# Kernel tuning notes

Hardware: AMD Instinct MI355X
Metric: run time of the kernel (lower is better)

The kernel has to match this reference:

```python
import jax, jax.numpy as jnp
import numpy as np

B, N, PREV, PRED, H = 16, 64, 6, 30, 256
E = N * (N - 1)
BN_EPS = 1e-5


def _mlp(x, W1, b1, W2, b2, gamma, beta):
    # Two-layer ELU MLP with batch norm over flattened (batch*rows) dim.
    h = jax.nn.elu(x @ W1 + b1)
    h = jax.nn.elu(h @ W2 + b2)
    b, n, d = h.shape
    f = h.reshape(b * n, d)
    mu = f.mean(axis=0)
    var = f.var(axis=0)
    f = (f - mu) * jax.lax.rsqrt(var + BN_EPS) * gamma + beta
    return f.reshape(b, n, d)


def setup_inputs() -> dict:
    key = jax.random.key(0)
    ks = jax.random.split(key, 8)
    # fully-connected directed graph without self loops
    recv, send = np.where(~np.eye(N, dtype=bool))  # each [E]
    rel_rec = jnp.broadcast_to(jax.nn.one_hot(jnp.asarray(recv), N)[None], (B, E, N)).astype(jnp.float32)
    rel_send = jnp.broadcast_to(jax.nn.one_hot(jnp.asarray(send), N)[None], (B, E, N)).astype(jnp.float32)

    def xavier(k, shape):
        fan_in, fan_out = shape
        std = np.sqrt(2.0 / (fan_in + fan_out))
        return jax.random.normal(k, shape, jnp.float32) * std

    return {
        "prev_actor_centers": jax.random.normal(ks[0], (B, N, PREV, 2), jnp.float32) * 10.0,
        "rel_rec": rel_rec,
        "rel_send": rel_send,
        "W_traj": xavier(ks[1], (PREV * 2, H)),
        "b_traj": jnp.full((H,), 0.1, jnp.float32),
        "n2e_W1": xavier(ks[2], (2 * H, H)),
        "n2e_b1": jnp.full((H,), 0.1, jnp.float32),
        "n2e_W2": xavier(ks[3], (H, H)),
        "n2e_b2": jnp.full((H,), 0.1, jnp.float32),
        "n2e_gamma": jnp.ones((H,), jnp.float32),
        "n2e_beta": jnp.zeros((H,), jnp.float32),
        "e2n_W1": xavier(ks[4], (2 * H, H)),
        "e2n_b1": jnp.full((H,), 0.1, jnp.float32),
        "e2n_W2": xavier(ks[5], (H, H)),
        "e2n_b2": jnp.full((H,), 0.1, jnp.float32),
        "e2n_gamma": jnp.ones((H,), jnp.float32),
        "e2n_beta": jnp.zeros((H,), jnp.float32),
        "W_fuse": xavier(ks[6], (2 * H, H)),
        "b_fuse": jnp.full((H,), 0.1, jnp.float32),
        "W_pred": xavier(ks[7], (H, PRED * 2)),
        "b_pred": jnp.full((PRED * 2,), 0.1, jnp.float32),
    }


def reference(prev_actor_centers, rel_rec, rel_send,
              W_traj, b_traj,
              n2e_W1, n2e_b1, n2e_W2, n2e_b2, n2e_gamma, n2e_beta,
              e2n_W1, e2n_b1, e2n_W2, e2n_b2, e2n_gamma, e2n_beta,
              W_fuse, b_fuse, W_pred, b_pred):
    b, n, prev, _ = prev_actor_centers.shape
    # relative displacements, first step zero
    diffs = prev_actor_centers[:, :, 1:, :] - prev_actor_centers[:, :, :-1, :]
    rel_pos = jnp.concatenate([jnp.zeros((b, n, 1, 2), prev_actor_centers.dtype), diffs], axis=2)
    rel_pos = rel_pos.reshape(b, n, prev * 2)
    x = rel_pos @ W_traj + b_traj  # [b, n, H] node features

    # node2edge: gather via one-hot relation matmuls
    receivers = jnp.einsum('ben,bnh->beh', rel_rec, x)
    senders = jnp.einsum('ben,bnh->beh', rel_send, x)
    edges = jnp.concatenate([receivers, senders], axis=-1)  # [b, E, 2H]
    e = _mlp(edges, n2e_W1, n2e_b1, n2e_W2, n2e_b2, n2e_gamma, n2e_beta)

    # edge2node: degree-normalized scatter via transposed relation matmuls
    deg_rec = rel_rec.sum(axis=1)  # [b, n]
    deg_rec = deg_rec + (deg_rec == 0).astype(deg_rec.dtype)
    incoming = jnp.einsum('ben,beh->bnh', rel_rec, e) / deg_rec[..., None]
    deg_send = rel_send.sum(axis=1)
    deg_send = deg_send + (deg_send == 0).astype(deg_send.dtype)
    outgoing = jnp.einsum('ben,beh->bnh', rel_send, e) / deg_send[..., None]
    nodes = jnp.concatenate([incoming, outgoing], axis=-1)  # [b, n, 2H]
    m = _mlp(nodes, e2n_W1, e2n_b1, e2n_W2, e2n_b2, e2n_gamma, e2n_beta)

    fused = jnp.concatenate([x, m], axis=-1) @ W_fuse + b_fuse  # [b, n, H]
    rel = fused @ W_pred + b_pred  # [b, n, PRED*2]

    current_loc = prev_actor_centers[:, :, -1, :]  # [b, n, 2]
    current_loc = jnp.broadcast_to(current_loc[:, :, None, :], (b, n, PRED, 2)).reshape(b, n, PRED * 2)
    pos = jnp.cumsum(rel.reshape(b, n, PRED, 2), axis=2).reshape(b, n, PRED * 2) + current_loc
    return (rel, pos)
```

## Files before the change

kernel.cpp:

```cpp
#include <hip/hip_runtime.h>
#include <hip/hip_bf16.h>

#define BB 16
#define NN 64
#define PREVN 6
#define PREDN 30
#define HH 256
#define EE 4032
#define EROWS (BB*EE)
#define NROWS (BB*NN)

typedef short short8 __attribute__((ext_vector_type(8)));
typedef float f32x4 __attribute__((ext_vector_type(4)));

enum : int {
  OFF_STATS_E = 0,
  OFF_STATS_M = 1024,
  OFF_XRS     = 2048,
  F32_END     = 264192
};
enum : size_t {
  BO_W1TE  = 0,
  BO_W2TE  = 131072,
  BO_W1TN  = 196608,
  BO_W2TN  = 327680,
  BO_WFT   = 393216,
  BO_WPT   = 524288,
  BO_XG    = 540672,
  BO_NODES = 802816,
  BO_H1G   = 1327104,
  BO_M2    = 1589248,
  BO_FG    = 1851392,
  BO_E2    = 2113536
};

__device__ __forceinline__ float eluf(float v) { return v > 0.f ? v : __expf(v) - 1.f; }

__device__ __forceinline__ float xembed(const float* __restrict__ centers,
                                        const float* __restrict__ Wt,
                                        const float* __restrict__ bt,
                                        int rr, int col) {
  const float* c = centers + rr * 12;
  float acc = bt[col];
  #pragma unroll
  for (int t = 0; t < 5; ++t) {
    float dx = c[(t+1)*2 + 0] - c[t*2 + 0];
    float dy = c[(t+1)*2 + 1] - c[t*2 + 1];
    acc += dx * Wt[(2 + 2*t)*HH + col] + dy * Wt[(3 + 2*t)*HH + col];
  }
  return acc;
}

struct PrepArgs {
  const float *centers, *W_traj, *b_traj;
  const float *n2e_W1, *n2e_W2, *e2n_W1, *e2n_W2, *W_fuse, *W_pred;
  float* ws;
  __hip_bfloat16 *w1te, *w2te, *w1tn, *w2tn, *wft, *wpt, *xg;
};

__global__ __launch_bounds__(256) void k_prep(PrepArgs a) {
  __shared__ float t[64][65];
  const int bid = blockIdx.x, tid = threadIdx.x;
  if (bid < 128) {
    const float* W; __hip_bfloat16* WT; int K, lb;
    if (bid < 32)      { W = a.n2e_W1; WT = a.w1te; K = 512; lb = bid; }
    else if (bid < 48) { W = a.n2e_W2; WT = a.w2te; K = 256; lb = bid - 32; }
    else if (bid < 80) { W = a.e2n_W1; WT = a.w1tn; K = 512; lb = bid - 48; }
    else if (bid < 96) { W = a.e2n_W2; WT = a.w2tn; K = 256; lb = bid - 80; }
    else               { W = a.W_fuse; WT = a.wft;  K = 512; lb = bid - 96; }
    int KB = K / 64;
    int k0 = (lb % KB) * 64, n0 = (lb / KB) * 64;
    int tx = tid & 63, ty = tid >> 6;
    #pragma unroll
    for (int i = 0; i < 16; ++i)
      t[ty + i*4][tx] = W[(size_t)(k0 + ty + i*4) * 256 + n0 + tx];
    __syncthreads();
    #pragma unroll
    for (int i = 0; i < 16; ++i)
      WT[(size_t)(n0 + ty + i*4) * K + k0 + tx] = __float2bfloat16(t[tx][ty + i*4]);
  } else if (bid < 192) {
    int idx = (bid - 128) * 256 + tid;
    int c = idx >> 8, k = idx & 255;
    a.wpt[idx] = __float2bfloat16(c < 60 ? a.W_pred[k * 60 + c] : 0.f);
  } else if (bid < 200) {
    a.ws[(bid - 192) * 256 + tid] = 0.f;
  } else {
    int row0 = (bid - 200) * 16;
    #pragma unroll
    for (int r = 0; r < 16; ++r)
      a.xg[(size_t)(row0 + r)*256 + tid] =
          __float2bfloat16(xembed(a.centers, a.W_traj, a.b_traj, row0 + r, tid));
  }
}

__global__ __launch_bounds__(64) void k_xrs2(
    const __hip_bfloat16* __restrict__ xg,
    const __hip_bfloat16* __restrict__ W1T,
    const float* __restrict__ b1,
    __hip_bfloat16* __restrict__ xrs) {
  const int lane = threadIdx.x;
  const int m16 = lane & 15, quad = lane >> 4;
  const int ko = quad * 8;
  const int rt = blockIdx.x >> 3, s = blockIdx.x & 7;
  const int half = s >> 2, j0 = (s & 3) * 64;
  const int row0 = rt * 16;
  __hip_bfloat16* dst = xrs + (size_t)half * 262144;

  f32x4 acc[4];
  #pragma unroll
  for (int jt = 0; jt < 4; ++jt) {
    float bv = half ? 0.f : b1[j0 + jt*16 + m16];
    acc[jt] = (f32x4){bv, bv, bv, bv};
  }
  #pragma unroll
  for (int ks = 0; ks < 8; ++ks) {
    short8 af = *reinterpret_cast<const short8*>(
        xg + (size_t)(row0 + m16)*256 + ks*32 + ko);
    short8 bf[4];
    #pragma unroll
    for (int jt = 0; jt < 4; ++jt)
      bf[jt] = *reinterpret_cast<const short8*>(
          W1T + (size_t)(j0 + jt*16 + m16)*512 + half*256 + ks*32 + ko);
    #pragma unroll
    for (int jt = 0; jt < 4; ++jt)
      acc[jt] = __builtin_amdgcn_mfma_f32_16x16x32_bf16(af, bf[jt], acc[jt], 0, 0, 0);
  }
  #pragma unroll
  for (int jt = 0; jt < 4; ++jt)
    #pragma unroll
    for (int r = 0; r < 4; ++r)
      dst[(size_t)(row0 + quad*4 + r)*256 + j0 + jt*16 + m16] =
          __float2bfloat16(acc[jt][r]);
}

__global__ __launch_bounds__(256, 4) void k_mlp6(
    const __hip_bfloat16* __restrict__ xrs,
    const __hip_bfloat16* __restrict__ W2T,
    const float* __restrict__ b2,
    __hip_bfloat16* __restrict__ outp,
    float* __restrict__ stats) {
  __shared__ alignas(16) __hip_bfloat16 h1s[64][264];
  __shared__ float sst[2][256];
  __shared__ int sd64[64];
  __shared__ int rcf[64];
  const int tid = threadIdx.x;
  const int w = tid >> 6, lane = tid & 63;
  const int m16 = lane & 15, quad = lane >> 4;
  const int ko = quad * 8;
  const int blk = blockIdx.x;
  const int bb = blk / 63, lb = blk - bb*63;
  const int row0 = blk * 64;
  const int n0 = (lb * 64) / 63;
  const int colw = w * 64;

  if (tid < 64) {
    int e = lb*64 + tid;
    int rc = e / 63; int jj = e - rc*63;
    sd64[tid] = jj + (jj >= rc ? 1 : 0);
    rcf[tid]  = rc - n0;
  }
  sst[0][tid] = 0.f;
  sst[1][tid] = 0.f;
  __syncthreads();

  {
    const int ty = tid >> 7;
    const int c2 = (tid & 127) * 2;
    const __hip_bfloat16* xrb = xrs + (size_t)(bb*64 + n0)*256 + c2;
    const __hip_bfloat16* xsb = xrs + 262144 + (size_t)bb*64*256 + c2;
    #pragma unroll 4
    for (int r2 = 0; r2 < 32; ++r2) {
      int r = ty*32 + r2;
      __hip_bfloat162 xa = *reinterpret_cast<const __hip_bfloat162*>(
          xrb + (size_t)rcf[r]*256);
      __hip_bfloat162 xs2 = *reinterpret_cast<const __hip_bfloat162*>(
          xsb + (size_t)sd64[r]*256);
      __hip_bfloat162 o;
      o.x = __float2bfloat16(eluf(__bfloat162float(xa.x) + __bfloat162float(xs2.x)));
      o.y = __float2bfloat16(eluf(__bfloat162float(xa.y) + __bfloat162float(xs2.y)));
      *reinterpret_cast<__hip_bfloat162*>(&h1s[r][c2]) = o;
    }
  }
  __syncthreads();

  f32x4 acc2[4][4];
  #pragma unroll
  for (int jt = 0; jt < 4; ++jt) {
    float bv = b2[colw + jt*16 + m16];
    #pragma unroll
    for (int mt = 0; mt < 4; ++mt) acc2[mt][jt] = (f32x4){bv, bv, bv, bv};
  }
  #pragma unroll
  for (int kt = 0; kt < 4; ++kt) {
    #pragma unroll
    for (int ks = 0; ks < 2; ++ks) {
      const int k0 = kt*64 + ks*32 + ko;
      short8 af[4], bf[4];
      #pragma unroll
      for (int jt = 0; jt < 4; ++jt)
        bf[jt] = *reinterpret_cast<const short8*>(
            W2T + (size_t)(colw + jt*16 + m16)*256 + k0);
      #pragma unroll
      for (int mt = 0; mt < 4; ++mt)
        af[mt] = *(const short8*)((const char*)h1s +
                     (size_t)(mt*16 + m16)*528 + k0*2);
      #pragma unroll
      for (int mt = 0; mt < 4; ++mt)
        #pragma unroll
        for (int jt = 0; jt < 4; ++jt)
          acc2[mt][jt] = __builtin_amdgcn_mfma_f32_16x16x32_bf16(af[mt], bf[jt],
                                                                 acc2[mt][jt], 0, 0, 0);
    }
  }
  __syncthreads();

  #pragma unroll
  for (int jt = 0; jt < 4; ++jt) {
    float ps = 0.f, pq = 0.f;
    #pragma unroll
    for (int mt = 0; mt < 4; ++mt)
      #pragma unroll
      for (int r = 0; r < 4; ++r) {
        float hv = eluf(acc2[mt][jt][r]);
        h1s[mt*16 + quad*4 + r][colw + jt*16 + m16] = __float2bfloat16(hv);
        ps += hv; pq += hv * hv;
      }
    atomicAdd(&sst[0][colw + jt*16 + m16], ps);
    atomicAdd(&sst[1][colw + jt*16 + m16], pq);
  }
  __syncthreads();

  atomicAdd(&stats[tid], sst[0][tid]);
  atomicAdd(&stats[256 + tid], sst[1][tid]);
  #pragma unroll
  for (int i = 0; i < 8; ++i) {
    int u = i*256 + tid;
    int r = u >> 5, c = (u & 31) * 8;
    *reinterpret_cast<uint4*>(outp + (size_t)(row0 + r)*HH + c) =
        *reinterpret_cast<const uint4*>(&h1s[r][c]);
  }
}

__global__ __launch_bounds__(1024) void k_agg2(const __hip_bfloat16* __restrict__ e2,
                                               const float* __restrict__ st,
                                               const float* __restrict__ gam,
                                               const float* __restrict__ bet,
                                               __hip_bfloat16* __restrict__ nodes) {
  __shared__ float red[32][256];
  const int blk = blockIdx.x;
  const int bn = blk >> 1, half = blk & 1;
  const int b = bn >> 6, n = bn & 63;
  const int tid = threadIdx.x;
  const int c8 = (tid & 31) * 8;
  const int rg = tid >> 5;
  const __hip_bfloat16* base = e2 + (size_t)b * EE * HH;
  float s[8] = {0.f,0.f,0.f,0.f,0.f,0.f,0.f,0.f};
  for (int j = rg; j < 63; j += 32) {
    const __hip_bfloat16* rp;
    if (half == 0) {
      rp = base + (size_t)(n*63 + j)*HH;
    } else {
      int i = j + (j >= n ? 1 : 0);
      int e = i*63 + n - (n > i ? 1 : 0);
      rp = base + (size_t)e*HH;
    }
    union { uint4 u; __hip_bfloat16 h[8]; } v;
    v.u = *reinterpret_cast<const uint4*>(rp + c8);
    #pragma unroll
    for (int jj = 0; jj < 8; ++jj) s[jj] += __bfloat162float(v.h[jj]);
  }
  #pragma unroll
  for (int jj = 0; jj < 8; jj += 4)
    *reinterpret_cast<float4*>(&red[rg][c8 + jj]) =
        (float4){s[jj], s[jj+1], s[jj+2], s[jj+3]};
  __syncthreads();
  if (tid < 256) {
    float S = 0.f;
    #pragma unroll
    for (int r = 0; r < 32; ++r) S += red[r][tid];
    const float inv = 1.f / (float)EROWS;
    float mean = st[tid] * inv;
    float var  = fmaxf(st[256 + tid] * inv - mean*mean, 0.f);
    float a = gam[tid] * rsqrtf(var + 1e-5f);
    float c0 = bet[tid] - mean * a;
    nodes[(size_t)bn*512 + half*256 + tid] = __float2bfloat16(a * S * (1.f/63.f) + c0);
  }
}

__global__ __launch_bounds__(64) void k_n1(
    const __hip_bfloat16* __restrict__ nodes,
    const __hip_bfloat16* __restrict__ W1T,
    const float* __restrict__ b1,
    __hip_bfloat16* __restrict__ h1g) {
  __shared__ alignas(16) __hip_bfloat16 hls[16][40];
  const int lane = threadIdx.x;
  const int m16 = lane & 15, quad = lane >> 4;
  const int ko = quad * 8;
  const int row0 = (blockIdx.x >> 3) * 16;
  const int j0 = (blockIdx.x & 7) * 32;

  f32x4 acc[2];
  #pragma unroll
  for (int jt = 0; jt < 2; ++jt) {
    float bv = b1[j0 + jt*16 + m16];
    acc[jt] = (f32x4){bv, bv, bv, bv};
  }
  #pragma unroll
  for (int ks = 0; ks < 16; ++ks) {
    short8 af = *reinterpret_cast<const short8*>(
        nodes + (size_t)(row0 + m16)*512 + ks*32 + ko);
    short8 bf[2];
    #pragma unroll
    for (int jt = 0; jt < 2; ++jt)
      bf[jt] = *reinterpret_cast<const short8*>(
          W1T + (size_t)(j0 + jt*16 + m16)*512 + ks*32 + ko);
    #pragma unroll
    for (int jt = 0; jt < 2; ++jt)
      acc[jt] = __builtin_amdgcn_mfma_f32_16x16x32_bf16(af, bf[jt], acc[jt], 0, 0, 0);
  }
  #pragma unroll
  for (int jt = 0; jt < 2; ++jt)
    #pragma unroll
    for (int r = 0; r < 4; ++r)
      hls[quad*4 + r][jt*16 + m16] = __float2bfloat16(eluf(acc[jt][r]));
  {
    int r = lane >> 2, c = (lane & 3) * 8;
    *reinterpret_cast<uint4*>(h1g + (size_t)(row0 + r)*256 + j0 + c) =
        *reinterpret_cast<const uint4*>(&hls[r][c]);
  }
}

__global__ __launch_bounds__(64) void k_n2(
    const __hip_bfloat16* __restrict__ h1g,
    const __hip_bfloat16* __restrict__ W2T,
    const float* __restrict__ b2,
    __hip_bfloat16* __restrict__ m2,
    float* __restrict__ stats) {
  __shared__ alignas(16) __hip_bfloat16 hls[16][40];
  __shared__ float sst[2][32];
  const int lane = threadIdx.x;
  const int m16 = lane & 15, quad = lane >> 4;
  const int ko = quad * 8;
  const int row0 = (blockIdx.x >> 3) * 16;
  const int j0 = (blockIdx.x & 7) * 32;

  if (lane < 32) { sst[0][lane] = 0.f; sst[1][lane] = 0.f; }

  f32x4 acc[2];
  #pragma unroll
  for (int jt = 0; jt < 2; ++jt) {
    float bv = b2[j0 + jt*16 + m16];
    acc[jt] = (f32x4){bv, bv, bv, bv};
  }
  #pragma unroll
  for (int ks = 0; ks < 8; ++ks) {
    short8 af = *reinterpret_cast<const short8*>(
        h1g + (size_t)(row0 + m16)*256 + ks*32 + ko);
    short8 bf[2];
    #pragma unroll
    for (int jt = 0; jt < 2; ++jt)
      bf[jt] = *reinterpret_cast<const short8*>(
          W2T + (size_t)(j0 + jt*16 + m16)*256 + ks*32 + ko);
    #pragma unroll
    for (int jt = 0; jt < 2; ++jt)
      acc[jt] = __builtin_amdgcn_mfma_f32_16x16x32_bf16(af, bf[jt], acc[jt], 0, 0, 0);
  }
  #pragma unroll
  for (int jt = 0; jt < 2; ++jt) {
    float ps = 0.f, pq = 0.f;
    #pragma unroll
    for (int r = 0; r < 4; ++r) {
      float hv = eluf(acc[jt][r]);
      hls[quad*4 + r][jt*16 + m16] = __float2bfloat16(hv);
      ps += hv; pq += hv * hv;
    }
    atomicAdd(&sst[0][jt*16 + m16], ps);
    atomicAdd(&sst[1][jt*16 + m16], pq);
  }
  if (lane < 32) {
    atomicAdd(&stats[j0 + lane], sst[0][lane]);
    atomicAdd(&stats[256 + j0 + lane], sst[1][lane]);
  }
  {
    int r = lane >> 2, c = (lane & 3) * 8;
    *reinterpret_cast<uint4*>(m2 + (size_t)(row0 + r)*256 + j0 + c) =
        *reinterpret_cast<const uint4*>(&hls[r][c]);
  }
}

__global__ __launch_bounds__(64) void k_hf(
    const __hip_bfloat16* __restrict__ xg,
    const __hip_bfloat16* __restrict__ m2,
    const float* __restrict__ stM,
    const float* __restrict__ gam,
    const float* __restrict__ bet,
    const __hip_bfloat16* __restrict__ WfT,
    const float* __restrict__ bfv,
    __hip_bfloat16* __restrict__ fg) {
  __shared__ alignas(16) __hip_bfloat16 hls[16][40];
  __shared__ float bnA[256], bnC[256];
  const int lane = threadIdx.x;
  const int m16 = lane & 15, quad = lane >> 4;
  const int ko = quad * 8;
  const int row0 = (blockIdx.x >> 3) * 16;
  const int j0 = (blockIdx.x & 7) * 32;

  {
    const float inv = 1.f / (float)NROWS;
    #pragma unroll
    for (int j = 0; j < 4; ++j) {
      int k = lane*4 + j;
      float mean = stM[k] * inv;
      float var  = fmaxf(stM[256 + k] * inv - mean*mean, 0.f);
      float am = gam[k] * rsqrtf(var + 1e-5f);
      bnA[k] = am;
      bnC[k] = bet[k] - mean * am;
    }
  }

  f32x4 acc[2];
  #pragma unroll
  for (int jt = 0; jt < 2; ++jt) {
    float bv = bfv[j0 + jt*16 + m16];
    acc[jt] = (f32x4){bv, bv, bv, bv};
  }
  #pragma unroll
  for (int ks = 0; ks < 16; ++ks) {
    short8 af;
    if (ks < 8) {
      af = *reinterpret_cast<const short8*>(
          xg + (size_t)(row0 + m16)*256 + ks*32 + ko);
    } else {
      int k0 = (ks - 8)*32 + ko;
      union { uint4 u; __hip_bfloat16 h[8]; } v;
      v.u = *reinterpret_cast<const uint4*>(m2 + (size_t)(row0 + m16)*256 + k0);
      union { short8 s8; __hip_bfloat16 h[8]; } o;
      #pragma unroll
      for (int j = 0; j < 8; ++j)
        o.h[j] = __float2bfloat16(bnA[k0+j] * __bfloat162float(v.h[j]) + bnC[k0+j]);
      af = o.s8;
    }
    short8 bf[2];
    #pragma unroll
    for (int jt = 0; jt < 2; ++jt)
      bf[jt] = *reinterpret_cast<const short8*>(
          WfT + (size_t)(j0 + jt*16 + m16)*512 + ks*32 + ko);
    #pragma unroll
    for (int jt = 0; jt < 2; ++jt)
      acc[jt] = __builtin_amdgcn_mfma_f32_16x16x32_bf16(af, bf[jt], acc[jt], 0, 0, 0);
  }
  #pragma unroll
  for (int jt = 0; jt < 2; ++jt)
    #pragma unroll
    for (int r = 0; r < 4; ++r)
      hls[quad*4 + r][jt*16 + m16] = __float2bfloat16(acc[jt][r]);
  {
    int r = lane >> 2, c = (lane & 3) * 8;
    *reinterpret_cast<uint4*>(fg + (size_t)(row0 + r)*256 + j0 + c) =
        *reinterpret_cast<const uint4*>(&hls[r][c]);
  }
}

__global__ __launch_bounds__(64) void k_pred(
    const __hip_bfloat16* __restrict__ fg,
    const __hip_bfloat16* __restrict__ WpT,
    const float* __restrict__ bp,
    const float* __restrict__ centers,
    float* __restrict__ out) {
  __shared__ float rl[16][68];
  const int lane = threadIdx.x;
  const int m16 = lane & 15, quad = lane >> 4;
  const int ko = quad * 8;
  const int row0 = blockIdx.x * 16;

  f32x4 acc[4];
  #pragma unroll
  for (int jt = 0; jt < 4; ++jt) {
    int c = jt*16 + m16;
    float bv = (c < 60) ? bp[c] : 0.f;
    acc[jt] = (f32x4){bv, bv, bv, bv};
  }
  #pragma unroll
  for (int ks = 0; ks < 8; ++ks) {
    short8 af = *reinterpret_cast<const short8*>(
        fg + (size_t)(row0 + m16)*256 + ks*32 + ko);
    short8 bf[4];
    #pragma unroll
    for (int jt = 0; jt < 4; ++jt)
      bf[jt] = *reinterpret_cast<const short8*>(
          WpT + (size_t)(jt*16 + m16)*256 + ks*32 + ko);
    #pragma unroll
    for (int jt = 0; jt < 4; ++jt)
      acc[jt] = __builtin_amdgcn_mfma_f32_16x16x32_bf16(af, bf[jt], acc[jt], 0, 0, 0);
  }
  #pragma unroll
  for (int jt = 0; jt < 4; ++jt) {
    int c = jt*16 + m16;
    #pragma unroll
    for (int r = 0; r < 4; ++r) {
      int lr = quad*4 + r;
      rl[lr][c] = acc[jt][r];
      if (c < 60) out[(size_t)(row0 + lr)*60 + c] = acc[jt][r];
    }
  }
  if (lane < 32) {
    int lr = lane >> 1, xy = lane & 1;
    int grow = row0 + lr;
    float run = centers[(size_t)(grow*PREVN + 5)*2 + xy];
    #pragma unroll
    for (int p = 0; p < PREDN; ++p) {
      run += rl[lr][2*p + xy];
      out[61440 + (size_t)grow*60 + 2*p + xy] = run;
    }
  }
}

extern "C" void kernel_launch(void* const* d_in, const int* in_sizes, int n_in,
                              void* d_out, int out_size, void* d_ws, size_t ws_size,
                              hipStream_t stream) {
  const float* centers = (const float*)d_in[0];
  float* ws = (float*)d_ws;
  __hip_bfloat16* wb = (__hip_bfloat16*)(ws + F32_END);
  __hip_bfloat16* xrs = (__hip_bfloat16*)(ws + OFF_XRS);

  const float* W_traj = (const float*)d_in[3];
  const float* b_traj = (const float*)d_in[4];
  const float* n2e_b1 = (const float*)d_in[6];
  const float* n2e_b2 = (const float*)d_in[8];
  const float* n2e_g  = (const float*)d_in[9];
  const float* n2e_be = (const float*)d_in[10];
  const float* e2n_b1 = (const float*)d_in[12];
  const float* e2n_b2 = (const float*)d_in[14];
  const float* e2n_g  = (const float*)d_in[15];
  const float* e2n_be = (const float*)d_in[16];
  const float* b_fuse = (const float*)d_in[18];
  const float* b_pred = (const float*)d_in[20];

  PrepArgs pa;
  pa.centers = centers; pa.W_traj = W_traj; pa.b_traj = b_traj;
  pa.n2e_W1 = (const float*)d_in[5];  pa.n2e_W2 = (const float*)d_in[7];
  pa.e2n_W1 = (const float*)d_in[11]; pa.e2n_W2 = (const float*)d_in[13];
  pa.W_fuse = (const float*)d_in[17]; pa.W_pred = (const float*)d_in[19];
  pa.ws = ws;
  pa.w1te = wb + BO_W1TE; pa.w2te = wb + BO_W2TE;
  pa.w1tn = wb + BO_W1TN; pa.w2tn = wb + BO_W2TN;
  pa.wft = wb + BO_WFT;   pa.wpt = wb + BO_WPT;
  pa.xg = wb + BO_XG;

  k_prep<<<264, 256, 0, stream>>>(pa);
  k_xrs2<<<512, 64, 0, stream>>>(wb + BO_XG, wb + BO_W1TE, n2e_b1, xrs);
  k_mlp6<<<EROWS/64, 256, 0, stream>>>(xrs, wb + BO_W2TE, n2e_b2, wb + BO_E2,
                                       ws + OFF_STATS_E);
  k_agg2<<<2*NROWS, 1024, 0, stream>>>(wb + BO_E2, ws + OFF_STATS_E, n2e_g, n2e_be,
                                       wb + BO_NODES);
  k_n1<<<512, 64, 0, stream>>>(wb + BO_NODES, wb + BO_W1TN, e2n_b1, wb + BO_H1G);
  k_n2<<<512, 64, 0, stream>>>(wb + BO_H1G, wb + BO_W2TN, e2n_b2, wb + BO_M2,
                               ws + OFF_STATS_M);
  k_hf<<<512, 64, 0, stream>>>(wb + BO_XG, wb + BO_M2, ws + OFF_STATS_M,
                               e2n_g, e2n_be, wb + BO_WFT, b_fuse, wb + BO_FG);
  k_pred<<<64, 64, 0, stream>>>(wb + BO_FG, wb + BO_WPT, b_pred, centers,
                                (float*)d_out);
}
```

Baseline: 200.0 us.

## Fuse incoming-edge aggregation into edge MLP epilogue and vectorize gather

Edge blocks in the edge-MLP kernel now keep per-receiver partial sums of their outputs, split at the boundary between the two receiver nodes each 64-row tile covers. These are atomically added into a zeroed fp32 buffer, so the aggregation kernel only gathers the strided sender-side rows and uses smaller blocks. The h1 gather also changes from bf16x2 loads with index tables in shared memory to uint4 loads with indices computed inline. The cost is extra global atomics plus a zeroing pass in the prep kernel. The buffer is aliased onto the H1G region, which is written later.

```diff
diff --git a/kernel.cpp b/kernel.cpp
--- a/kernel.cpp
+++ b/kernel.cpp
@@ -55,6 +55,7 @@
   const float *centers, *W_traj, *b_traj;
   const float *n2e_W1, *n2e_W2, *e2n_W1, *e2n_W2, *W_fuse, *W_pred;
   float* ws;
+  float* inc;
   __hip_bfloat16 *w1te, *w2te, *w1tn, *w2tn, *wft, *wpt, *xg;
 };
 
@@ -84,12 +85,17 @@
     a.wpt[idx] = __float2bfloat16(c < 60 ? a.W_pred[k * 60 + c] : 0.f);
   } else if (bid < 200) {
     a.ws[(bid - 192) * 256 + tid] = 0.f;
-  } else {
+  } else if (bid < 264) {
     int row0 = (bid - 200) * 16;
     #pragma unroll
     for (int r = 0; r < 16; ++r)
       a.xg[(size_t)(row0 + r)*256 + tid] =
           __float2bfloat16(xembed(a.centers, a.W_traj, a.b_traj, row0 + r, tid));
+  } else {
+    float* p = a.inc + (size_t)(bid - 264) * 4096;
+    #pragma unroll
+    for (int i = 0; i < 4; ++i)
+      *reinterpret_cast<float4*>(p + (i*256 + tid)*4) = (float4){0.f,0.f,0.f,0.f};
   }
 }
 
@@ -133,16 +139,15 @@
           __float2bfloat16(acc[jt][r]);
 }
 
-__global__ __launch_bounds__(256, 4) void k_mlp6(
+__global__ __launch_bounds__(256, 4) void k_mlp7(
     const __hip_bfloat16* __restrict__ xrs,
     const __hip_bfloat16* __restrict__ W2T,
     const float* __restrict__ b2,
     __hip_bfloat16* __restrict__ outp,
-    float* __restrict__ stats) {
+    float* __restrict__ stats,
+    float* __restrict__ incraw) {
   __shared__ alignas(16) __hip_bfloat16 h1s[64][264];
-  __shared__ float sst[2][256];
-  __shared__ int sd64[64];
-  __shared__ int rcf[64];
+  __shared__ float sst[3][256];
   const int tid = threadIdx.x;
   const int w = tid >> 6, lane = tid & 63;
   const int m16 = lane & 15, quad = lane >> 4;
@@ -151,34 +156,35 @@
   const int bb = blk / 63, lb = blk - bb*63;
   const int row0 = blk * 64;
   const int n0 = (lb * 64) / 63;
+  const int thr = (n0 + 1) * 63 - lb * 64;
   const int colw = w * 64;
 
-  if (tid < 64) {
-    int e = lb*64 + tid;
-    int rc = e / 63; int jj = e - rc*63;
-    sd64[tid] = jj + (jj >= rc ? 1 : 0);
-    rcf[tid]  = rc - n0;
-  }
-  sst[0][tid] = 0.f;
-  sst[1][tid] = 0.f;
-  __syncthreads();
+  #pragma unroll
+  for (int i = 0; i < 3; ++i) sst[i][tid] = 0.f;
 
   {
-    const int ty = tid >> 7;
-    const int c2 = (tid & 127) * 2;
-    const __hip_bfloat16* xrb = xrs + (size_t)(bb*64 + n0)*256 + c2;
-    const __hip_bfloat16* xsb = xrs + 262144 + (size_t)bb*64*256 + c2;
-    #pragma unroll 4
-    for (int r2 = 0; r2 < 32; ++r2) {
-      int r = ty*32 + r2;
-      __hip_bfloat162 xa = *reinterpret_cast<const __hip_bfloat162*>(
-          xrb + (size_t)rcf[r]*256);
-      __hip_bfloat162 xs2 = *reinterpret_cast<const __hip_bfloat162*>(
-          xsb + (size_t)sd64[r]*256);
-      __hip_bfloat162 o;
-      o.x = __float2bfloat16(eluf(__bfloat162float(xa.x) + __bfloat162float(xs2.x)));
-      o.y = __float2bfloat16(eluf(__bfloat162float(xa.y) + __bfloat162float(xs2.y)));
-      *reinterpret_cast<__hip_bfloat162*>(&h1s[r][c2]) = o;
+    const int rg = tid >> 5;
+    const int c8 = (tid & 31) * 8;
+    const __hip_bfloat16* xrb = xrs + (size_t)(bb*64 + n0)*256 + c8;
+    const __hip_bfloat16* xsb = xrs + 262144 + (size_t)bb*64*256 + c8;
+    union { uint4 u; __hip_bfloat16 h[8]; } vr0, vr1;
+    vr0.u = *reinterpret_cast<const uint4*>(xrb);
+    vr1.u = *reinterpret_cast<const uint4*>(xrb + 256);
+    #pragma unroll
+    for (int i = 0; i < 8; ++i) {
+      int r = rg + i*8;
+      int isn1 = (r >= thr) ? 1 : 0;
+      int rc = n0 + isn1;
+      int jj = lb*64 + r - rc*63;
+      int sd = jj + (jj >= rc ? 1 : 0);
+      union { uint4 u; __hip_bfloat16 h[8]; } vs, va, o;
+      vs.u = *reinterpret_cast<const uint4*>(xsb + (size_t)sd*256);
+      va.u = isn1 ? vr1.u : vr0.u;
+      #pragma unroll
+      for (int j = 0; j < 8; ++j)
+        o.h[j] = __float2bfloat16(eluf(__bfloat162float(va.h[j]) +
+                                       __bfloat162float(vs.h[j])));
+      *reinterpret_cast<uint4*>(&h1s[r][c8]) = o.u;
     }
   }
   __syncthreads();
@@ -216,22 +222,31 @@
 
   #pragma unroll
   for (int jt = 0; jt < 4; ++jt) {
-    float ps = 0.f, pq = 0.f;
+    float s0 = 0.f, s1 = 0.f, sq = 0.f;
     #pragma unroll
     for (int mt = 0; mt < 4; ++mt)
       #pragma unroll
       for (int r = 0; r < 4; ++r) {
+        int row = mt*16 + quad*4 + r;
         float hv = eluf(acc2[mt][jt][r]);
-        h1s[mt*16 + quad*4 + r][colw + jt*16 + m16] = __float2bfloat16(hv);
-        ps += hv; pq += hv * hv;
+        h1s[row][colw + jt*16 + m16] = __float2bfloat16(hv);
+        float t1 = (row >= thr) ? hv : 0.f;
+        s1 += t1; s0 += hv - t1;
+        sq += hv * hv;
       }
-    atomicAdd(&sst[0][colw + jt*16 + m16], ps);
-    atomicAdd(&sst[1][colw + jt*16 + m16], pq);
+    atomicAdd(&sst[0][colw + jt*16 + m16], s0);
+    atomicAdd(&sst[1][colw + jt*16 + m16], s1);
+    atomicAdd(&sst[2][colw + jt*16 + m16], sq);
   }
   __syncthreads();
 
-  atomicAdd(&stats[tid], sst[0][tid]);
-  atomicAdd(&stats[256 + tid], sst[1][tid]);
+  {
+    float s0 = sst[0][tid], s1 = sst[1][tid];
+    atomicAdd(&stats[tid], s0 + s1);
+    atomicAdd(&stats[256 + tid], sst[2][tid]);
+    atomicAdd(&incraw[(size_t)(bb*64 + n0)*256 + tid], s0);
+    atomicAdd(&incraw[(size_t)(bb*64 + n0 + 1)*256 + tid], s1);
+  }
   #pragma unroll
   for (int i = 0; i < 8; ++i) {
     int u = i*256 + tid;
@@ -241,31 +256,25 @@
   }
 }
 
-__global__ __launch_bounds__(1024) void k_agg2(const __hip_bfloat16* __restrict__ e2,
-                                               const float* __restrict__ st,
-                                               const float* __restrict__ gam,
-                                               const float* __restrict__ bet,
-                                               __hip_bfloat16* __restrict__ nodes) {
-  __shared__ float red[32][256];
-  const int blk = blockIdx.x;
-  const int bn = blk >> 1, half = blk & 1;
+__global__ __launch_bounds__(256) void k_aggS(const __hip_bfloat16* __restrict__ e2,
+                                              const float* __restrict__ incraw,
+                                              const float* __restrict__ st,
+                                              const float* __restrict__ gam,
+                                              const float* __restrict__ bet,
+                                              __hip_bfloat16* __restrict__ nodes) {
+  __shared__ float red[8][256];
+  const int bn = blockIdx.x;
   const int b = bn >> 6, n = bn & 63;
   const int tid = threadIdx.x;
   const int c8 = (tid & 31) * 8;
   const int rg = tid >> 5;
   const __hip_bfloat16* base = e2 + (size_t)b * EE * HH;
   float s[8] = {0.f,0.f,0.f,0.f,0.f,0.f,0.f,0.f};
-  for (int j = rg; j < 63; j += 32) {
-    const __hip_bfloat16* rp;
-    if (half == 0) {
-      rp = base + (size_t)(n*63 + j)*HH;
-    } else {
-      int i = j + (j >= n ? 1 : 0);
-      int e = i*63 + n - (n > i ? 1 : 0);
-      rp = base + (size_t)e*HH;
-    }
+  for (int j = rg; j < 63; j += 8) {
+    int i = j + (j >= n ? 1 : 0);
+    int e = i*63 + n - (n > i ? 1 : 0);
     union { uint4 u; __hip_bfloat16 h[8]; } v;
-    v.u = *reinterpret_cast<const uint4*>(rp + c8);
+    v.u = *reinterpret_cast<const uint4*>(base + (size_t)e*HH + c8);
     #pragma unroll
     for (int jj = 0; jj < 8; ++jj) s[jj] += __bfloat162float(v.h[jj]);
   }
@@ -274,17 +283,18 @@
     *reinterpret_cast<float4*>(&red[rg][c8 + jj]) =
         (float4){s[jj], s[jj+1], s[jj+2], s[jj+3]};
   __syncthreads();
-  if (tid < 256) {
-    float S = 0.f;
-    #pragma unroll
-    for (int r = 0; r < 32; ++r) S += red[r][tid];
-    const float inv = 1.f / (float)EROWS;
-    float mean = st[tid] * inv;
-    float var  = fmaxf(st[256 + tid] * inv - mean*mean, 0.f);
-    float a = gam[tid] * rsqrtf(var + 1e-5f);
-    float c0 = bet[tid] - mean * a;
-    nodes[(size_t)bn*512 + half*256 + tid] = __float2bfloat16(a * S * (1.f/63.f) + c0);
-  }
+  float S = 0.f;
+  #pragma unroll
+  for (int r = 0; r < 8; ++r) S += red[r][tid];
+  const float inv = 1.f / (float)EROWS;
+  float mean = st[tid] * inv;
+  float var  = fmaxf(st[256 + tid] * inv - mean*mean, 0.f);
+  float a = gam[tid] * rsqrtf(var + 1e-5f);
+  float c0 = bet[tid] - mean * a;
+  float in_v  = a * (incraw[(size_t)bn*256 + tid] * (1.f/63.f)) + c0;
+  float out_v = a * (S * (1.f/63.f)) + c0;
+  nodes[(size_t)bn*512 + tid]       = __float2bfloat16(in_v);
+  nodes[(size_t)bn*512 + 256 + tid] = __float2bfloat16(out_v);
 }
 
 __global__ __launch_bounds__(64) void k_n1(
@@ -522,6 +532,7 @@
   float* ws = (float*)d_ws;
   __hip_bfloat16* wb = (__hip_bfloat16*)(ws + F32_END);
   __hip_bfloat16* xrs = (__hip_bfloat16*)(ws + OFF_XRS);
+  float* incraw = (float*)(wb + BO_H1G);
 
   const float* W_traj = (const float*)d_in[3];
   const float* b_traj = (const float*)d_in[4];
@@ -541,18 +552,18 @@
   pa.n2e_W1 = (const float*)d_in[5];  pa.n2e_W2 = (const float*)d_in[7];
   pa.e2n_W1 = (const float*)d_in[11]; pa.e2n_W2 = (const float*)d_in[13];
   pa.W_fuse = (const float*)d_in[17]; pa.W_pred = (const float*)d_in[19];
-  pa.ws = ws;
+  pa.ws = ws; pa.inc = incraw;
   pa.w1te = wb + BO_W1TE; pa.w2te = wb + BO_W2TE;
   pa.w1tn = wb + BO_W1TN; pa.w2tn = wb + BO_W2TN;
   pa.wft = wb + BO_WFT;   pa.wpt = wb + BO_WPT;
   pa.xg = wb + BO_XG;
 
-  k_prep<<<264, 256, 0, stream>>>(pa);
+  k_prep<<<328, 256, 0, stream>>>(pa);
   k_xrs2<<<512, 64, 0, stream>>>(wb + BO_XG, wb + BO_W1TE, n2e_b1, xrs);
-  k_mlp6<<<EROWS/64, 256, 0, stream>>>(xrs, wb + BO_W2TE, n2e_b2, wb + BO_E2,
-                                       ws + OFF_STATS_E);
-  k_agg2<<<2*NROWS, 1024, 0, stream>>>(wb + BO_E2, ws + OFF_STATS_E, n2e_g, n2e_be,
-                                       wb + BO_NODES);
+  k_mlp7<<<EROWS/64, 256, 0, stream>>>(xrs, wb + BO_W2TE, n2e_b2, wb + BO_E2,
+                                       ws + OFF_STATS_E, incraw);
+  k_aggS<<<NROWS, 256, 0, stream>>>(wb + BO_E2, incraw, ws + OFF_STATS_E,
+                                    n2e_g, n2e_be, wb + BO_NODES);
   k_n1<<<512, 64, 0, stream>>>(wb + BO_NODES, wb + BO_W1TN, e2n_b1, wb + BO_H1G);
   k_n2<<<512, 64, 0, stream>>>(wb + BO_H1G, wb + BO_W2TN, e2n_b2, wb + BO_M2,
                                ws + OFF_STATS_M);
```

After: 201.8 us. About the same (+0.9%).
